# Kernel tuning notes

Hardware: AMD Instinct MI355X
Metric: run time of the kernel (lower is better)

The kernel has to match this reference:

```python
import jax, jax.numpy as jnp
import numpy as np

B, S, E, H, N = 16384, 256, 128, 128, 34  # batch, state_dim, reduced_lang_dim, mlp hidden, N_task
TEMP = 0.1
EPS = 1e-8  # torch cosine_similarity eps


def setup_inputs() -> dict:
    key = jax.random.key(0)
    ks = jax.random.split(key, 12)
    sc = 0.05
    return {
        "state": jax.random.normal(ks[0], (B, S), dtype=jnp.float32),
        "task_id": jax.random.randint(ks[1], (B,), 0, N),
        "prior": jax.random.normal(ks[2], (B, N), dtype=jnp.float32),
        # stacked weights of the 34 per-task MLPs (Linear(S,H) -> ReLU -> Linear(H,H) -> ReLU -> Linear(H,E))
        "W1": jax.random.normal(ks[3], (N, S, H), dtype=jnp.float32) * sc,
        "b1": jax.random.normal(ks[4], (N, H), dtype=jnp.float32) * sc,
        "W2": jax.random.normal(ks[5], (N, H, H), dtype=jnp.float32) * sc,
        "b2": jax.random.normal(ks[6], (N, H), dtype=jnp.float32) * sc,
        "W3": jax.random.normal(ks[7], (N, H, E), dtype=jnp.float32) * sc,
        "b3": jax.random.normal(ks[8], (N, E), dtype=jnp.float32) * sc,
        "lang_emb": jax.random.normal(ks[9], (N, E), dtype=jnp.float32),
    }


def reference(state, task_id, prior, W1, b1, W2, b2, W3, b3, lang_emb):
    # 34 parallel MLPs as a single batched GEMM stack: [B,S] x [N,S,H] -> [B,N,H]
    h = jax.nn.relu(jnp.einsum('bs,nsh->bnh', state, W1) + b1)
    h = jax.nn.relu(jnp.einsum('bnh,nhk->bnk', h, W2) + b2)
    q = jnp.einsum('bnk,nke->bne', h, W3) + b3            # [B,N,E]
    # normalize (torch.norm division, no eps, then cosine_similarity renormalizes -> unit)
    q = q / jnp.linalg.norm(q, axis=-1, keepdims=True)
    lang = lang_emb[task_id]                              # [B,E]
    lang_n = lang / jnp.maximum(jnp.linalg.norm(lang, axis=-1, keepdims=True), EPS)
    cos_sim = jnp.einsum('bne,be->bn', q, lang_n)         # [B,N]
    log_task_prob = jax.nn.log_softmax(cos_sim / TEMP, axis=-1)
    task_prob_prior = jax.nn.softmax(prior, axis=-1)      # exp(log_softmax(prior))
    latent_vec = jnp.einsum('bne,bn->be', q, task_prob_prior)
    latent_target = jax.lax.stop_gradient(q[jnp.arange(B), task_id])  # detach
    rep_vec = jnp.concatenate([state, latent_vec], axis=-1)           # [B, S+E]
    return rep_vec, log_task_prob, latent_target, latent_vec
```

## Files before the change

kernel.cpp:

```cpp
#include <hip/hip_runtime.h>
#include <hip/hip_bf16.h>
#include <hip/hip_fp16.h>
#include <cstdint>
#include <cstddef>

typedef __bf16 bf16;
typedef __attribute__((ext_vector_type(8))) __bf16 bf16x8;
typedef __attribute__((ext_vector_type(16))) float f32x16;

static_assert(sizeof(bf16x8) == 16, "bf16x8 must be 16B");

#define NTASK 34
#define BTOT 16384
#define WSTRIDE 73728

__device__ __forceinline__ f32x16 mfma32(bf16x8 a, bf16x8 b, f32x16 c) {
  return __builtin_amdgcn_mfma_f32_32x32x16_bf16(a, b, c, 0, 0, 0);
}

__device__ __forceinline__ void gload_lds16(const void* g, void* l) {
  __builtin_amdgcn_global_load_lds((__attribute__((address_space(1))) void*)g,
                                   (__attribute__((address_space(3))) void*)l,
                                   16, 0, 0);
}

__device__ __forceinline__ unsigned pack2(float lo, float hi) {
  union { __bf16 h[2]; unsigned u; } v;
  v.h[0] = (__bf16)lo; v.h[1] = (__bf16)hi;
  return v.u;
}

__device__ __forceinline__ void pl32swap(unsigned &a, unsigned &b) {
  asm volatile("v_permlane32_swap_b32 %0, %1" : "+v"(a), "+v"(b));
}

__global__ void prep_all(const float* __restrict__ W1, const float* __restrict__ W2,
                         const float* __restrict__ W3, const float* __restrict__ b1,
                         const float* __restrict__ b2, const float* __restrict__ b3,
                         const float* __restrict__ state, const float* __restrict__ prior,
                         bf16* __restrict__ wdst, bf16* __restrict__ sdst,
                         float* __restrict__ ppt) {
  int bid = blockIdx.x;
  if (bid < 1224) {
    int idx = bid * 256 + threadIdx.x;
    int n = idx / 9216;
    int r = idx - n * 9216;
    int g = r >> 8;
    int m = (r >> 6) & 3;
    int l = r & 63;
    int col = m * 32 + (l & 31);
    int kj = (l >> 5) << 3;
    bf16x8 v;
#pragma unroll
    for (int j = 0; j < 8; ++j) v[j] = (bf16)0.f;
    if (g < 16) {
      const float* s = W1 + ((size_t)n * 256 + g * 16 + kj) * 128 + col;
#pragma unroll
      for (int j = 0; j < 8; ++j) v[j] = (bf16)s[(size_t)j * 128];
    } else if (g == 16) {
      if (l < 32) v[0] = (bf16)b1[n * 128 + col];
    } else if (g == 17) {
    } else if (g < 26) {
      const float* s = W2 + ((size_t)n * 128 + (g - 18) * 16 + kj) * 128 + col;
#pragma unroll
      for (int j = 0; j < 8; ++j) v[j] = (bf16)s[(size_t)j * 128];
    } else if (g == 26) {
      if (l < 32) v[0] = (bf16)b2[n * 128 + col];
    } else if (g < 35) {
      const float* s = W3 + ((size_t)n * 128 + (g - 27) * 16 + kj) * 128 + col;
#pragma unroll
      for (int j = 0; j < 8; ++j) v[j] = (bf16)s[(size_t)j * 128];
    } else {
      if (l < 32) v[0] = (bf16)b3[n * 128 + col];
    }
    *(bf16x8*)(wdst + (size_t)n * WSTRIDE + (size_t)(g * 4 + m) * 512 + l * 8) = v;
  } else if (bid < 3272) {
    int idx = (bid - 1224) * 256 + threadIdx.x;
    int rb = idx >> 10;
    int r = idx & 1023;
    int ks = r >> 6;
    int l = r & 63;
    int b = rb * 32 + (l & 31);
    int k0 = ks * 16 + ((l >> 5) << 3);
    const float* s = state + (size_t)b * 256 + k0;
    bf16x8 v;
#pragma unroll
    for (int j = 0; j < 8; ++j) v[j] = (bf16)s[j];
    *(bf16x8*)(sdst + (size_t)(rb * 16 + ks) * 512 + l * 8) = v;
  } else {
    int row = (bid - 3272) * 4 + (threadIdx.x >> 6);
    int lane = threadIdx.x & 63;
    float v = (lane < NTASK) ? prior[(size_t)row * NTASK + lane] : -INFINITY;
    float m = v;
#pragma unroll
    for (int mm = 1; mm < 64; mm <<= 1) m = fmaxf(m, __shfl_xor(m, mm));
    float e = (lane < NTASK) ? expf(v - m) : 0.0f;
    float s = e;
#pragma unroll
    for (int mm = 1; mm < 64; mm <<= 1) s += __shfl_xor(s, mm);
    if (lane < NTASK) ppt[(size_t)lane * BTOT + row] = e / s;
  }
}

__global__ void prep_langn(const float* __restrict__ lang, float* __restrict__ out) {
  __shared__ float red[2];
  int n = blockIdx.x;
  int t = threadIdx.x;
  float v = lang[(size_t)n * 128 + t];
  float ss = v * v;
#pragma unroll
  for (int m = 1; m < 64; m <<= 1) ss += __shfl_xor(ss, m);
  if ((t & 63) == 0) red[t >> 6] = ss;
  __syncthreads();
  float s = red[0] + red[1];
  float sc = 1.0f / fmaxf(sqrtf(s), 1e-8f);
  out[(size_t)n * 128 + t] = v * sc;
}


__global__ void __launch_bounds__(256, 2)
pass1_kernel(const int* __restrict__ task_id, const bf16* __restrict__ wstream,
             const bf16* __restrict__ sf, const float* __restrict__ langn,
             const float* __restrict__ pp_t,
             float* __restrict__ cs_t, __half* __restrict__ lat_part,
             float* __restrict__ out_tgt) {
  __shared__ __align__(16) bf16 shW[3 * 8192];

  const int tid = threadIdx.x;
  const int l = tid & 63;
  const int wid = tid >> 6;
  const int hi = l >> 5;
  const int b = l & 31;
  const int tg = blockIdx.x >> 7;
  const int rg = blockIdx.x & 127;
  const int start = (tg < 2) ? tg * 9 : (18 + (tg - 2) * 8);
  const int cnt = (tg < 2) ? 9 : 8;
  const int nwin = cnt * 9;
  const int row0 = rg * 128 + wid * 32 + b;
  const int rb0 = rg * 4 + wid;

  const int tidn = task_id[row0];
  const bf16* sb = sf + (size_t)rb0 * 8192 + l * 8;
  const bf16* wsrc = wstream + (size_t)start * WSTRIDE;

#define STAGE_WIN(slot, w) \
  { _Pragma("unroll") \
    for (int c = 0; c < 4; ++c) \
      gload_lds16(wsrc + (size_t)(w) * 8192 + c * 2048 + tid * 8, \
                  shW + (slot) * 8192 + c * 2048 + tid * 8); }

#define WIN_TOP() \
  { asm volatile("s_waitcnt vmcnt(4)" ::: "memory"); \
    __builtin_amdgcn_s_barrier(); }

#define KMFMA(slot, gi, bop) \
  { _Pragma("unroll") \
    for (int mt = 0; mt < 4; ++mt) { \
      bf16x8 wf = *(const bf16x8*)(shW + (slot) * 8192 + ((gi) * 4 + mt) * 512 + l * 8); \
      acc[mt] = mfma32(wf, (bop), acc[mt]); } }

  STAGE_WIN(0, 0);
  STAGE_WIN(1, 1);
  bf16x8 sring[16];
#pragma unroll
  for (int i = 0; i < 16; ++i) sring[i] = *(const bf16x8*)(sb + i * 512);

  union { unsigned u[4]; bf16x8 v; } cf;
  cf.u[0] = (l < 32) ? 0x3f80u : 0u;
  cf.u[1] = 0u; cf.u[2] = 0u; cf.u[3] = 0u;

  f32x16 z;
#pragma unroll
  for (int i = 0; i < 16; ++i) z[i] = 0.f;
  f32x16 lat[4] = {z, z, z, z};

  auto transition = [&](f32x16* acc, bf16x8* f) {
#pragma unroll
    for (int mt = 0; mt < 4; ++mt) {
      unsigned p[8];
#pragma unroll
      for (int q = 0; q < 4; ++q) {
        p[2 * q]     = pack2(fmaxf(acc[mt][4 * q + 0], 0.f), fmaxf(acc[mt][4 * q + 1], 0.f));
        p[2 * q + 1] = pack2(fmaxf(acc[mt][4 * q + 2], 0.f), fmaxf(acc[mt][4 * q + 3], 0.f));
      }
      pl32swap(p[0], p[2]); pl32swap(p[1], p[3]);
      pl32swap(p[4], p[6]); pl32swap(p[5], p[7]);
      union { unsigned u[4]; bf16x8 v; } e, o;
      e.u[0] = p[0]; e.u[1] = p[1]; e.u[2] = p[2]; e.u[3] = p[3];
      o.u[0] = p[4]; o.u[1] = p[5]; o.u[2] = p[6]; o.u[3] = p[7];
      f[2 * mt] = e.v; f[2 * mt + 1] = o.v;
    }
  };

  for (int t = 0; t < cnt; ++t) {
    const int n = start + t;
    const int w0g = t * 9;
    f32x16 acc[4];
    bf16x8 f2[8], f3[8];

    WIN_TOP();
    if (w0g + 2 < nwin) STAGE_WIN(2, w0g + 2);
#pragma unroll
    for (int mt = 0; mt < 4; ++mt) acc[mt] = z;
    __builtin_amdgcn_s_setprio(1);
#pragma unroll
    for (int gi = 0; gi < 4; ++gi) KMFMA(0, gi, sring[gi]);
    __builtin_amdgcn_s_setprio(0);

    WIN_TOP();
    if (w0g + 3 < nwin) STAGE_WIN(0, w0g + 3);
    __builtin_amdgcn_s_setprio(1);
#pragma unroll
    for (int gi = 0; gi < 4; ++gi) KMFMA(1, gi, sring[4 + gi]);
    __builtin_amdgcn_s_setprio(0);

    WIN_TOP();
    if (w0g + 4 < nwin) STAGE_WIN(1, w0g + 4);
    __builtin_amdgcn_s_setprio(1);
#pragma unroll
    for (int gi = 0; gi < 4; ++gi) KMFMA(2, gi, sring[8 + gi]);
    __builtin_amdgcn_s_setprio(0);

    WIN_TOP();
    if (w0g + 5 < nwin) STAGE_WIN(2, w0g + 5);
    __builtin_amdgcn_s_setprio(1);
#pragma unroll
    for (int gi = 0; gi < 4; ++gi) KMFMA(0, gi, sring[12 + gi]);
    __builtin_amdgcn_s_setprio(0);

    WIN_TOP();
    if (w0g + 6 < nwin) STAGE_WIN(0, w0g + 6);
    __builtin_amdgcn_s_setprio(1);
    KMFMA(1, 0, cf.v);
    __builtin_amdgcn_s_setprio(0);
    transition(acc, f2);
#pragma unroll
    for (int mt = 0; mt < 4; ++mt) acc[mt] = z;
    __builtin_amdgcn_s_setprio(1);
    KMFMA(1, 2, f2[0]);
    KMFMA(1, 3, f2[1]);
    __builtin_amdgcn_s_setprio(0);

    WIN_TOP();
    if (w0g + 7 < nwin) STAGE_WIN(1, w0g + 7);
    __builtin_amdgcn_s_setprio(1);
#pragma unroll
    for (int gi = 0; gi < 4; ++gi) KMFMA(2, gi, f2[2 + gi]);
    __builtin_amdgcn_s_setprio(0);

    WIN_TOP();
    if (w0g + 8 < nwin) STAGE_WIN(2, w0g + 8);
    __builtin_amdgcn_s_setprio(1);
    KMFMA(0, 0, f2[6]);
    KMFMA(0, 1, f2[7]);
    KMFMA(0, 2, cf.v);
    __builtin_amdgcn_s_setprio(0);
    transition(acc, f3);
#pragma unroll
    for (int mt = 0; mt < 4; ++mt) acc[mt] = z;
    __builtin_amdgcn_s_setprio(1);
    KMFMA(0, 3, f3[0]);
    __builtin_amdgcn_s_setprio(0);

    WIN_TOP();
    if (w0g + 9 < nwin) STAGE_WIN(0, w0g + 9);
    __builtin_amdgcn_s_setprio(1);
#pragma unroll
    for (int gi = 0; gi < 4; ++gi) KMFMA(1, gi, f3[1 + gi]);
    __builtin_amdgcn_s_setprio(0);

    WIN_TOP();
    if (w0g + 10 < nwin) STAGE_WIN(1, w0g + 10);
    __builtin_amdgcn_s_setprio(1);
    KMFMA(2, 0, f3[5]);
    KMFMA(2, 1, f3[6]);
    KMFMA(2, 2, f3[7]);
    KMFMA(2, 3, cf.v);
    __builtin_amdgcn_s_setprio(0);

    float ssq = 0.f, dot = 0.f;
    const float* lgb = langn + (size_t)tidn * 128;
#pragma unroll
    for (int mt = 0; mt < 4; ++mt)
#pragma unroll
      for (int q = 0; q < 4; ++q) {
        int c0 = mt * 32 + q * 8 + 4 * hi;
        float4 lg = *(const float4*)(lgb + c0);
        float a0 = acc[mt][4 * q + 0], a1 = acc[mt][4 * q + 1];
        float a2 = acc[mt][4 * q + 2], a3 = acc[mt][4 * q + 3];
        ssq += a0 * a0 + a1 * a1 + a2 * a2 + a3 * a3;
        dot += a0 * lg.x + a1 * lg.y + a2 * lg.z + a3 * lg.w;
      }
    ssq += __shfl_xor(ssq, 32);
    dot += __shfl_xor(dot, 32);
    float inv = rsqrtf(ssq);
    if (l < 32) cs_t[(size_t)row0 * NTASK + n] = dot * inv;
    float pwi = pp_t[(size_t)n * BTOT + row0] * inv;
#pragma unroll
    for (int mt = 0; mt < 4; ++mt) lat[mt] += acc[mt] * pwi;
    if (tidn == n) {
#pragma unroll
      for (int mt = 0; mt < 4; ++mt)
#pragma unroll
        for (int q = 0; q < 4; ++q) {
          float4 qv = {acc[mt][4 * q + 0] * inv, acc[mt][4 * q + 1] * inv,
                       acc[mt][4 * q + 2] * inv, acc[mt][4 * q + 3] * inv};
          *(float4*)(out_tgt + (size_t)row0 * 128 + mt * 32 + q * 8 + 4 * hi) = qv;
        }
    }
  }

  __half* lp = lat_part + ((size_t)tg * BTOT + row0) * 128;
#pragma unroll
  for (int mt = 0; mt < 4; ++mt)
#pragma unroll
    for (int q = 0; q < 4; ++q) {
      int c0 = mt * 32 + q * 8 + 4 * hi;
      union { __half h[4]; uint2 u; } v;
      v.h[0] = __float2half(lat[mt][4 * q + 0]);
      v.h[1] = __float2half(lat[mt][4 * q + 1]);
      v.h[2] = __float2half(lat[mt][4 * q + 2]);
      v.h[3] = __float2half(lat[mt][4 * q + 3]);
      *(uint2*)(lp + c0) = v.u;
    }
#undef STAGE_WIN
#undef WIN_TOP
#undef KMFMA
}


__global__ void __launch_bounds__(256)
pass3_kernel(const float* __restrict__ state, const float* __restrict__ cs_t,
             const __half* __restrict__ lat_part,
             float* __restrict__ out_rep, float* __restrict__ out_ltp,
             float* __restrict__ out_lat) {
  int w = threadIdx.x >> 6, l = threadIdx.x & 63;
  size_t row = (size_t)blockIdx.x * 4 + w;

  float c = (l < NTASK) ? cs_t[row * NTASK + l] * 10.0f : -1e30f;
  float cm = c;
#pragma unroll
  for (int mm = 1; mm < 64; mm <<= 1) cm = fmaxf(cm, __shfl_xor(cm, mm));
  float ce = (l < NTASK) ? expf(c - cm) : 0.0f;
  float cs = ce;
#pragma unroll
  for (int mm = 1; mm < 64; mm <<= 1) cs += __shfl_xor(cs, mm);
  if (l < NTASK) out_ltp[row * NTASK + l] = c - cm - logf(cs);

  float2 lv = {0.f, 0.f};
#pragma unroll
  for (int g = 0; g < 4; ++g) {
    __half2 p = *(const __half2*)(lat_part + ((size_t)g * BTOT + row) * 128 + 2 * l);
    lv.x += __low2float(p);
    lv.y += __high2float(p);
  }
  *(float2*)(out_lat + row * 128 + 2 * l) = lv;
  *(float2*)(out_rep + row * 384 + 256 + 2 * l) = lv;

  float4 sv = *(const float4*)(state + row * 256 + l * 4);
  *(float4*)(out_rep + row * 384 + l * 4) = sv;
}


extern "C" void kernel_launch(void* const* d_in, const int* in_sizes, int n_in,
                              void* d_out, int out_size, void* d_ws, size_t ws_size,
                              hipStream_t stream) {
  (void)in_sizes; (void)n_in; (void)out_size; (void)ws_size;
  const float* state = (const float*)d_in[0];
  const int* task_id = (const int*)d_in[1];
  const float* prior = (const float*)d_in[2];
  const float* W1 = (const float*)d_in[3];
  const float* b1 = (const float*)d_in[4];
  const float* W2 = (const float*)d_in[5];
  const float* b2 = (const float*)d_in[6];
  const float* W3 = (const float*)d_in[7];
  const float* b3 = (const float*)d_in[8];
  const float* lang = (const float*)d_in[9];

  char* ws = (char*)d_ws;
  bf16* wstream  = (bf16*)(ws + 0);
  bf16* sf       = (bf16*)(ws + 5013504);
  float* langn   = (float*)(ws + 13402112);
  float* pp_t    = (float*)(ws + 13419520);
  float* cs_t    = (float*)(ws + 15647744);
  __half* lat_part = (__half*)(ws + 17875968);

  float* out = (float*)d_out;
  float* out_rep = out;
  float* out_ltp = out + 6291456;
  float* out_tgt = out + 6848512;
  float* out_lat = out + 8945664;

  prep_all<<<7368, 256, 0, stream>>>(W1, W2, W3, b1, b2, b3, state, prior,
                                     wstream, sf, pp_t);
  prep_langn<<<NTASK, 128, 0, stream>>>(lang, langn);
  pass1_kernel<<<512, 256, 0, stream>>>(task_id, wstream, sf, langn, pp_t,
                                        cs_t, lat_part, out_tgt);
  pass3_kernel<<<4096, 256, 0, stream>>>(state, cs_t, lat_part,
                                         out_rep, out_ltp, out_lat);
}
```

Before: 133.6 us.

## Accumulate latent in packed half2 and interleave task-group block order

Two separate changes. The per-row latent accumulator now lives as packed fp16 half2 values updated with hfma2, which halves the registers it needs (64 fp32 down to 32 packed) to ease register pressure at two blocks per CU. The block-index mapping also changes so that neighbouring blocks cover different task groups for adjacent row groups, which alters L2 reuse of the streamed weights and the state. Accumulating in fp16 across up to nine tasks loses precision and could push the latent output outside tolerance.

```diff
diff --git a/kernel.cpp b/kernel.cpp
--- a/kernel.cpp
+++ b/kernel.cpp
@@ -131,8 +131,9 @@
   const int wid = tid >> 6;
   const int hi = l >> 5;
   const int b = l & 31;
-  const int tg = blockIdx.x >> 7;
-  const int rg = blockIdx.x & 127;
+  const int bid = blockIdx.x;
+  const int tg = (bid & 7) >> 1;
+  const int rg = ((bid >> 3) << 1) | (bid & 1);
   const int start = (tg < 2) ? tg * 9 : (18 + (tg - 2) * 8);
   const int cnt = (tg < 2) ? 9 : 8;
   const int nwin = cnt * 9;
@@ -172,7 +173,13 @@
   f32x16 z;
 #pragma unroll
   for (int i = 0; i < 16; ++i) z[i] = 0.f;
-  f32x16 lat[4] = {z, z, z, z};
+
+  const __half2 hz = __float2half2_rn(0.0f);
+  __half2 lat[4][4][2];
+#pragma unroll
+  for (int mt = 0; mt < 4; ++mt)
+#pragma unroll
+    for (int q = 0; q < 4; ++q) { lat[mt][q][0] = hz; lat[mt][q][1] = hz; }
 
   auto transition = [&](f32x16* acc, bf16x8* f) {
 #pragma unroll
@@ -296,8 +303,16 @@
     float inv = rsqrtf(ssq);
     if (l < 32) cs_t[(size_t)row0 * NTASK + n] = dot * inv;
     float pwi = pp_t[(size_t)n * BTOT + row0] * inv;
-#pragma unroll
-    for (int mt = 0; mt < 4; ++mt) lat[mt] += acc[mt] * pwi;
+    __half2 pw2 = __float2half2_rn(pwi);
+#pragma unroll
+    for (int mt = 0; mt < 4; ++mt)
+#pragma unroll
+      for (int q = 0; q < 4; ++q) {
+        lat[mt][q][0] = __hfma2(__floats2half2_rn(acc[mt][4 * q + 0], acc[mt][4 * q + 1]),
+                                pw2, lat[mt][q][0]);
+        lat[mt][q][1] = __hfma2(__floats2half2_rn(acc[mt][4 * q + 2], acc[mt][4 * q + 3]),
+                                pw2, lat[mt][q][1]);
+      }
     if (tidn == n) {
 #pragma unroll
       for (int mt = 0; mt < 4; ++mt)
@@ -316,11 +331,9 @@
 #pragma unroll
     for (int q = 0; q < 4; ++q) {
       int c0 = mt * 32 + q * 8 + 4 * hi;
-      union { __half h[4]; uint2 u; } v;
-      v.h[0] = __float2half(lat[mt][4 * q + 0]);
-      v.h[1] = __float2half(lat[mt][4 * q + 1]);
-      v.h[2] = __float2half(lat[mt][4 * q + 2]);
-      v.h[3] = __float2half(lat[mt][4 * q + 3]);
+      union { __half2 h[2]; uint2 u; } v;
+      v.h[0] = lat[mt][q][0];
+      v.h[1] = lat[mt][q][1];
       *(uint2*)(lp + c0) = v.u;
     }
 #undef STAGE_WIN
```

New measurement: 139.3 us. 4.2% more time.
